# Kernel tuning notes

Measured on AMD Instinct MI355X. Metric: run time of the kernel, lower is better.

Reference implementation:

```python
import jax, jax.numpy as jnp
import numpy as np
from jax import lax

B, S, H, T = 64, 512, 1024, 48


def setup_inputs() -> dict:
    key = jax.random.key(0)
    ks = jax.random.split(key, 8)
    x = jax.random.normal(ks[0], (B, S, H), dtype=jnp.float32)
    # left-aligned variable-length attention mask (lengths in [S//2, S])
    lengths = jax.random.randint(ks[1], (B,), S // 2, S + 1)
    attention_mask = (jnp.arange(S)[None, :] < lengths[:, None]).astype(jnp.int32)
    labels = jax.random.randint(ks[2], (B, S), 0, T).astype(jnp.int64)
    # decoder Linear(H, T)
    W = jax.random.normal(ks[3], (H, T), dtype=jnp.float32) / np.sqrt(H)
    b = jnp.zeros((T,), dtype=jnp.float32)
    # CRF parameters (allennlp-style: transitions + start/end transitions)
    transitions = jax.random.normal(ks[4], (T, T), dtype=jnp.float32) * 0.1
    start_trans = jax.random.normal(ks[5], (T,), dtype=jnp.float32) * 0.1
    end_trans = jax.random.normal(ks[6], (T,), dtype=jnp.float32) * 0.1
    return {"x": x, "attention_mask": attention_mask, "labels": labels,
            "W": W, "b": b, "transitions": transitions,
            "start_trans": start_trans, "end_trans": end_trans}


def _log_partition(logits, mask, trans, start, end):
    # logits [B,S,T], mask [B,S] int. Returns logZ [B].
    alpha0 = start[None, :] + logits[:, 0]                     # [B,T]
    emits = jnp.moveaxis(logits[:, 1:], 1, 0)                  # [S-1,B,T]
    ms = mask[:, 1:].T                                         # [S-1,B]

    def step(alpha, inp):
        emit, m = inp
        inner = alpha[:, :, None] + trans[None, :, :] + emit[:, None, :]  # [B,T,T]
        new = jax.nn.logsumexp(inner, axis=1)
        alpha = jnp.where(m[:, None] > 0, new, alpha)
        return alpha, None

    alpha, _ = lax.scan(step, alpha0, (emits, ms))
    return jax.nn.logsumexp(alpha + end[None, :], axis=1)      # [B]


def _gold_score(logits, labels, mask, trans, start, end):
    maskf = mask.astype(logits.dtype)
    emit = jnp.take_along_axis(logits, labels[..., None], axis=2)[..., 0]  # [B,S]
    emit_score = jnp.sum(emit * maskf, axis=1)
    tr = trans[labels[:, :-1], labels[:, 1:]]                   # [B,S-1]
    trans_score = jnp.sum(tr * maskf[:, 1:], axis=1)
    last_idx = jnp.sum(mask, axis=1) - 1                        # [B]
    last_tags = jnp.take_along_axis(labels, last_idx[:, None], axis=1)[:, 0]
    return start[labels[:, 0]] + emit_score + trans_score + end[last_tags]


def _viterbi(logits, mask, trans, start, end):
    Bn, Sn, Tn = logits.shape
    v0 = start[None, :] + logits[:, 0]
    emits = jnp.moveaxis(logits[:, 1:], 1, 0)                  # [S-1,B,T]
    ms = mask[:, 1:].T
    ident = jnp.broadcast_to(jnp.arange(Tn, dtype=jnp.int32)[None, :], (Bn, Tn))

    def step(v, inp):
        emit, m = inp
        scores = v[:, :, None] + trans[None, :, :]              # [B,T_prev,T_cur]
        bp = jnp.argmax(scores, axis=1).astype(jnp.int32)       # [B,T]
        best = jnp.max(scores, axis=1) + emit
        v_new = jnp.where(m[:, None] > 0, best, v)
        bp = jnp.where(m[:, None] > 0, bp, ident)               # identity at padded steps
        return v_new, bp

    v, bps = lax.scan(step, v0, (emits, ms))                    # bps [S-1,B,T]
    last = jnp.argmax(v + end[None, :], axis=1).astype(jnp.int32)  # [B]

    def back(tag, bp):
        prev = jnp.take_along_axis(bp, tag[:, None], axis=1)[:, 0]
        return prev, tag

    first_tag, rest = lax.scan(back, last, bps, reverse=True)   # rest [S-1,B]
    tags = jnp.concatenate([first_tag[:, None], rest.T], axis=1)  # [B,S]
    return (tags * mask).astype(jnp.int64)                      # pad with zeros


def reference(x, attention_mask, labels, W, b, transitions, start_trans, end_trans):
    features = jnp.einsum('bsh,ht->bst', x, W) + b              # decoder Linear
    pred_labels = _viterbi(features, attention_mask, transitions, start_trans, end_trans)
    logZ = _log_partition(features, attention_mask, transitions, start_trans, end_trans)
    gold = _gold_score(features, labels, attention_mask, transitions, start_trans, end_trans)
    loss = -jnp.sum(gold - logZ)                                # -log-likelihood, summed over batch
    return features, pred_labels, loss
```

## Files before the change

### kernel.cpp

```cpp
#include <hip/hip_runtime.h>
#include <hip/hip_bf16.h>
#include <math.h>

#define Bn 64
#define Sn 512
#define Hn 1024
#define Tn 48

#define LOG2E 1.4426950408889634f
#define LN2f  0.6931471805599453f

#define PRED_OFF (Bn*Sn*Tn)
#define LOSS_OFF (PRED_OFF + Bn*Sn)

#define RL(x,i) __int_as_float(__builtin_amdgcn_readlane(__float_as_int(x),(i)))

#if __has_builtin(__builtin_amdgcn_exp2f)
#define EXP2(x) __builtin_amdgcn_exp2f(x)
#else
#define EXP2(x) exp2f(x)
#endif
#if __has_builtin(__builtin_amdgcn_logf)
#define LOG2(x) __builtin_amdgcn_logf(x)
#else
#define LOG2(x) log2f(x)
#endif

#define DOT4(ACC,A,B) { ACC += (A).x*(B).x; ACC += (A).y*(B).y; ACC += (A).z*(B).z; ACC += (A).w*(B).w; }

__global__ __launch_bounds__(256) void gemm_feat(
    const float* __restrict__ x, const float* __restrict__ W,
    const float* __restrict__ bias, float* __restrict__ feat)
{
  __shared__ __align__(16) float xs[128][68];
  __shared__ __align__(16) float wsT[Tn][68];
  const int tid = threadIdx.x;
  const int tx = tid & 7;
  const int ty = tid >> 3;
  const size_t row0 = (size_t)blockIdx.x * 128;
  const int srr = tid >> 4;
  const int scc = (tid & 15) * 4;

  float4 xreg[8];
  float  wreg[12];
  #pragma unroll
  for (int p = 0; p < 8; ++p)
    xreg[p] = *reinterpret_cast<const float4*>(&x[(row0 + srr + p*16)*Hn + scc]);
  #pragma unroll
  for (int i = 0; i < 12; ++i) {
    const int id = tid + i*256; const int kk = id/Tn; const int t = id - kk*Tn;
    wreg[i] = W[(size_t)kk*Tn + t];
  }

  float acc[4][6];
  #pragma unroll
  for (int r = 0; r < 4; ++r)
    #pragma unroll
    for (int c = 0; c < 6; ++c) acc[r][c] = 0.f;

  for (int k0 = 0; k0 < Hn; k0 += 64) {
    #pragma unroll
    for (int p = 0; p < 8; ++p)
      *reinterpret_cast<float4*>(&xs[srr + p*16][scc]) = xreg[p];
    #pragma unroll
    for (int i = 0; i < 12; ++i) {
      const int id = tid + i*256; const int kk = id/Tn; const int t = id - kk*Tn;
      wsT[t][kk] = wreg[i];
    }
    __syncthreads();
    if (k0 + 64 < Hn) {
      #pragma unroll
      for (int p = 0; p < 8; ++p)
        xreg[p] = *reinterpret_cast<const float4*>(&x[(row0 + srr + p*16)*Hn + (k0+64) + scc]);
      #pragma unroll
      for (int i = 0; i < 12; ++i) {
        const int id = tid + i*256; const int kk = id/Tn; const int t = id - kk*Tn;
        wreg[i] = W[(size_t)(k0 + 64 + kk)*Tn + t];
      }
    }
    #pragma unroll 4
    for (int kk = 0; kk < 64; kk += 4) {
      const float4 a0 = *reinterpret_cast<const float4*>(&xs[ty*4+0][kk]);
      const float4 a1 = *reinterpret_cast<const float4*>(&xs[ty*4+1][kk]);
      const float4 a2 = *reinterpret_cast<const float4*>(&xs[ty*4+2][kk]);
      const float4 a3 = *reinterpret_cast<const float4*>(&xs[ty*4+3][kk]);
      const float4 w0 = *reinterpret_cast<const float4*>(&wsT[tx*6+0][kk]);
      const float4 w1 = *reinterpret_cast<const float4*>(&wsT[tx*6+1][kk]);
      const float4 w2 = *reinterpret_cast<const float4*>(&wsT[tx*6+2][kk]);
      const float4 w3 = *reinterpret_cast<const float4*>(&wsT[tx*6+3][kk]);
      const float4 w4 = *reinterpret_cast<const float4*>(&wsT[tx*6+4][kk]);
      const float4 w5 = *reinterpret_cast<const float4*>(&wsT[tx*6+5][kk]);
      DOT4(acc[0][0],a0,w0) DOT4(acc[0][1],a0,w1) DOT4(acc[0][2],a0,w2)
      DOT4(acc[0][3],a0,w3) DOT4(acc[0][4],a0,w4) DOT4(acc[0][5],a0,w5)
      DOT4(acc[1][0],a1,w0) DOT4(acc[1][1],a1,w1) DOT4(acc[1][2],a1,w2)
      DOT4(acc[1][3],a1,w3) DOT4(acc[1][4],a1,w4) DOT4(acc[1][5],a1,w5)
      DOT4(acc[2][0],a2,w0) DOT4(acc[2][1],a2,w1) DOT4(acc[2][2],a2,w2)
      DOT4(acc[2][3],a2,w3) DOT4(acc[2][4],a2,w4) DOT4(acc[2][5],a2,w5)
      DOT4(acc[3][0],a3,w0) DOT4(acc[3][1],a3,w1) DOT4(acc[3][2],a3,w2)
      DOT4(acc[3][3],a3,w3) DOT4(acc[3][4],a3,w4) DOT4(acc[3][5],a3,w5)
    }
    __syncthreads();
  }
  #pragma unroll
  for (int c = 0; c < 6; ++c) {
    const int col = tx*6 + c;
    const float bv = bias[col];
    #pragma unroll
    for (int r = 0; r < 4; ++r)
      feat[(row0 + ty*4 + r)*Tn + col] = acc[r][c] + bv;
  }
}

__global__ __launch_bounds__(64, 1) void crf_kernel(
    const float* __restrict__ feat,
    const int* __restrict__ mask,
    const int* __restrict__ labels,
    const float* __restrict__ trans,
    const float* __restrict__ startv,
    const float* __restrict__ endv,
    float* __restrict__ pred_out,
    float* __restrict__ wsLogZ,
    float* __restrict__ wsGold)
{
  __shared__ unsigned char bpL[Sn*64];
  __shared__ unsigned char predL[Sn];

  const int role = blockIdx.x >> 6;
  const int b    = blockIdx.x & 63;
  const int lane = threadIdx.x;
  const float* fb = feat + (size_t)b * Sn * Tn;

  int lc = 0;
  #pragma unroll
  for (int it = 0; it < Sn/64; ++it) lc += (mask[(size_t)b*Sn + it*64 + lane] != 0);
  #pragma unroll
  for (int off = 32; off; off >>= 1) lc += __shfl_xor(lc, off);
  const int len = lc;

  const int j = (lane < Tn) ? lane : (Tn - 1);

  if (role == 0) {
    float4 trT[12];
    #pragma unroll
    for (int k = 0; k < 12; ++k) {
      trT[k].x = trans[(4*k+0)*Tn + j] * LOG2E;
      trT[k].y = trans[(4*k+1)*Tn + j] * LOG2E;
      trT[k].z = trans[(4*k+2)*Tn + j] * LOG2E;
      trT[k].w = trans[(4*k+3)*Tn + j] * LOG2E;
    }
    const float a0 = (startv[j] + fb[j]) * LOG2E;
    float Zref = RL(a0, 0);
    float beta = a0 - Zref;
    float em_cur = fb[Tn + j];
    for (int t = 1; t < len; ++t) {
      const int tn = (t + 1 < len) ? (t + 1) : t;
      const float em_nxt = fb[(size_t)tn*Tn + j];
      float s0 = 0.f, s1 = 0.f, s2 = 0.f, s3 = 0.f;
      #pragma unroll
      for (int k = 0; k < 12; ++k) {
        s0 += EXP2(RL(beta, 4*k+0) + trT[k].x);
        s1 += EXP2(RL(beta, 4*k+1) + trT[k].y);
        s2 += EXP2(RL(beta, 4*k+2) + trT[k].z);
        s3 += EXP2(RL(beta, 4*k+3) + trT[k].w);
      }
      const float dj = LOG2((s0 + s1) + (s2 + s3)) + em_cur * LOG2E;
      const float d0 = RL(dj, 0);
      Zref += d0;
      beta = dj - d0;
      em_cur = em_nxt;
    }
    float fv = (lane < Tn) ? beta + endv[lane] * LOG2E : -INFINITY;
    float m = fv;
    #pragma unroll
    for (int off = 32; off; off >>= 1) m = fmaxf(m, __shfl_xor(m, off));
    float e = (lane < Tn) ? EXP2(fv - m) : 0.f;
    #pragma unroll
    for (int off = 32; off; off >>= 1) e += __shfl_xor(e, off);
    if (lane == 0) wsLogZ[b] = (Zref + m + LOG2(e)) * LN2f;

  } else if (role == 1) {
    float4 trR[12];
    #pragma unroll
    for (int k = 0; k < 12; ++k) {
      trR[k].x = trans[(4*k+0)*Tn + j];
      trR[k].y = trans[(4*k+1)*Tn + j];
      trR[k].z = trans[(4*k+2)*Tn + j];
      trR[k].w = trans[(4*k+3)*Tn + j];
    }
    float v = startv[j] + fb[j];
    float em_cur = fb[Tn + j];
    for (int t = 1; t < len; ++t) {
      const int tn = (t + 1 < len) ? (t + 1) : t;
      const float em_nxt = fb[(size_t)tn*Tn + j];
      float bestA = -INFINITY, bestB = -INFINITY;
      int idxA = 0, idxB = 0;
      #pragma unroll
      for (int k = 0; k < 12; ++k) {
        const float4 tr = trR[k];
        const float q0 = RL(v, 4*k+0) + tr.x;
        const float q1 = RL(v, 4*k+1) + tr.y;
        const float q2 = RL(v, 4*k+2) + tr.z;
        const float q3 = RL(v, 4*k+3) + tr.w;
        float gv = q0; int gi = 4*k;
        bool g1 = q1 > gv; gv = g1 ? q1 : gv; gi = g1 ? 4*k+1 : gi;
        bool g2 = q2 > gv; gv = g2 ? q2 : gv; gi = g2 ? 4*k+2 : gi;
        bool g3 = q3 > gv; gv = g3 ? q3 : gv; gi = g3 ? 4*k+3 : gi;
        if ((k & 1) == 0) { bool g = gv > bestA; bestA = g ? gv : bestA; idxA = g ? gi : idxA; }
        else              { bool g = gv > bestB; bestB = g ? gv : bestB; idxB = g ? gi : idxB; }
      }
      float best; int bidx;
      if (bestB > bestA || (bestB == bestA && idxB < idxA)) { best = bestB; bidx = idxB; }
      else                                                  { best = bestA; bidx = idxA; }
      bpL[t*64 + lane] = (unsigned char)bidx;
      v = best + em_cur;
      em_cur = em_nxt;
    }
    float fv = (lane < Tn) ? v + endv[lane] : -INFINITY;
    int fi = (lane < Tn) ? lane : 64;
    #pragma unroll
    for (int off = 32; off; off >>= 1) {
      const float ov = __shfl_xor(fv, off);
      const int   oi = __shfl_xor(fi, off);
      if (ov > fv || (ov == fv && oi < fi)) { fv = ov; fi = oi; }
    }
    __syncthreads();
    if (lane == 0) {
      int tag = fi;
      predL[len - 1] = (unsigned char)tag;
      for (int t = len - 1; t >= 1; --t) {
        tag = bpL[t*64 + tag];
        predL[t - 1] = (unsigned char)tag;
      }
    }
    __syncthreads();
    #pragma unroll
    for (int it = 0; it < Sn/64; ++it) {
      const int s = it*64 + lane;
      pred_out[(size_t)b*Sn + s] = (s < len) ? (float)predL[s] : 0.f;
    }

  } else {
    float g = 0.f;
    #pragma unroll
    for (int it = 0; it < Sn/64; ++it) {
      const int sg = it*64 + lane;
      if (sg < len) {
        const int la = labels[(size_t)b*Sn + sg];
        float e = fb[(size_t)sg*Tn + la];
        if (sg > 0) e += trans[labels[(size_t)b*Sn + sg - 1]*Tn + la];
        g += e;
      }
    }
    #pragma unroll
    for (int off = 32; off; off >>= 1) g += __shfl_xor(g, off);
    if (lane == 0) {
      g += startv[labels[(size_t)b*Sn]] + endv[labels[(size_t)b*Sn + len - 1]];
      wsGold[b] = g;
    }
  }
}

__global__ void loss_reduce(const float* __restrict__ wsLogZ,
                            const float* __restrict__ wsGold,
                            float* __restrict__ out)
{
  const int lane = threadIdx.x;
  float v = wsLogZ[lane] - wsGold[lane];
  #pragma unroll
  for (int off = 32; off; off >>= 1) v += __shfl_xor(v, off);
  if (lane == 0) out[0] = v;
}

extern "C" void kernel_launch(void* const* d_in, const int* in_sizes, int n_in,
                              void* d_out, int out_size, void* d_ws, size_t ws_size,
                              hipStream_t stream) {
  const float* x      = (const float*)d_in[0];
  const int*   mask   = (const int*)  d_in[1];
  const int*   labels = (const int*)  d_in[2];
  const float* W      = (const float*)d_in[3];
  const float* bias   = (const float*)d_in[4];
  const float* trans  = (const float*)d_in[5];
  const float* startv = (const float*)d_in[6];
  const float* endv   = (const float*)d_in[7];

  float* out  = (float*)d_out;
  float* feat = out;
  float* pred = out + PRED_OFF;
  float* loss = out + LOSS_OFF;
  float* wsLogZ = (float*)d_ws;
  float* wsGold = wsLogZ + 64;

  gemm_feat<<<(Bn*Sn)/128, 256, 0, stream>>>(x, W, bias, feat);
  crf_kernel<<<192, 64, 0, stream>>>(feat, mask, labels, trans, startv, endv, pred, wsLogZ, wsGold);
  loss_reduce<<<1, 64, 0, stream>>>(wsLogZ, wsGold, loss);
}
```

Measured before the change: 386.0 us.

## Rewrite feature GEMM split-K, use exp-domain forward, parallel Viterbi backtrace

```diff
diff --git a/kernel.cpp b/kernel.cpp
--- a/kernel.cpp
+++ b/kernel.cpp
@@ -26,89 +26,76 @@
 #define LOG2(x) log2f(x)
 #endif
 
-#define DOT4(ACC,A,B) { ACC += (A).x*(B).x; ACC += (A).y*(B).y; ACC += (A).z*(B).z; ACC += (A).w*(B).w; }
+template<int CTRL>
+__device__ __forceinline__ float dpp_add(float v) {
+  return v + __int_as_float(__builtin_amdgcn_update_dpp(
+      0, __float_as_int(v), CTRL, 0xf, 0xf, false));
+}
 
 __global__ __launch_bounds__(256) void gemm_feat(
     const float* __restrict__ x, const float* __restrict__ W,
     const float* __restrict__ bias, float* __restrict__ feat)
 {
-  __shared__ __align__(16) float xs[128][68];
-  __shared__ __align__(16) float wsT[Tn][68];
   const int tid = threadIdx.x;
-  const int tx = tid & 7;
-  const int ty = tid >> 3;
-  const size_t row0 = (size_t)blockIdx.x * 128;
-  const int srr = tid >> 4;
-  const int scc = (tid & 15) * 4;
-
-  float4 xreg[8];
-  float  wreg[12];
-  #pragma unroll
-  for (int p = 0; p < 8; ++p)
-    xreg[p] = *reinterpret_cast<const float4*>(&x[(row0 + srr + p*16)*Hn + scc]);
-  #pragma unroll
-  for (int i = 0; i < 12; ++i) {
-    const int id = tid + i*256; const int kk = id/Tn; const int t = id - kk*Tn;
-    wreg[i] = W[(size_t)kk*Tn + t];
-  }
-
-  float acc[4][6];
-  #pragma unroll
-  for (int r = 0; r < 4; ++r)
-    #pragma unroll
-    for (int c = 0; c < 6; ++c) acc[r][c] = 0.f;
+  const int klane = tid & 15;
+  const int cg = tid >> 4;
+  const int col0 = cg * 3;
+  const size_t row0 = (size_t)blockIdx.x * 16;
+
+  float acc[16][3];
+  #pragma unroll
+  for (int r = 0; r < 16; ++r) { acc[r][0]=0.f; acc[r][1]=0.f; acc[r][2]=0.f; }
+
+  const float* xb = x + row0 * Hn + klane * 4;
+  const float* wb = W + (size_t)(klane * 4) * Tn + col0;
 
   for (int k0 = 0; k0 < Hn; k0 += 64) {
-    #pragma unroll
-    for (int p = 0; p < 8; ++p)
-      *reinterpret_cast<float4*>(&xs[srr + p*16][scc]) = xreg[p];
-    #pragma unroll
-    for (int i = 0; i < 12; ++i) {
-      const int id = tid + i*256; const int kk = id/Tn; const int t = id - kk*Tn;
-      wsT[t][kk] = wreg[i];
-    }
-    __syncthreads();
-    if (k0 + 64 < Hn) {
-      #pragma unroll
-      for (int p = 0; p < 8; ++p)
-        xreg[p] = *reinterpret_cast<const float4*>(&x[(row0 + srr + p*16)*Hn + (k0+64) + scc]);
-      #pragma unroll
-      for (int i = 0; i < 12; ++i) {
-        const int id = tid + i*256; const int kk = id/Tn; const int t = id - kk*Tn;
-        wreg[i] = W[(size_t)(k0 + 64 + kk)*Tn + t];
-      }
-    }
-    #pragma unroll 4
-    for (int kk = 0; kk < 64; kk += 4) {
-      const float4 a0 = *reinterpret_cast<const float4*>(&xs[ty*4+0][kk]);
-      const float4 a1 = *reinterpret_cast<const float4*>(&xs[ty*4+1][kk]);
-      const float4 a2 = *reinterpret_cast<const float4*>(&xs[ty*4+2][kk]);
-      const float4 a3 = *reinterpret_cast<const float4*>(&xs[ty*4+3][kk]);
-      const float4 w0 = *reinterpret_cast<const float4*>(&wsT[tx*6+0][kk]);
-      const float4 w1 = *reinterpret_cast<const float4*>(&wsT[tx*6+1][kk]);
-      const float4 w2 = *reinterpret_cast<const float4*>(&wsT[tx*6+2][kk]);
-      const float4 w3 = *reinterpret_cast<const float4*>(&wsT[tx*6+3][kk]);
-      const float4 w4 = *reinterpret_cast<const float4*>(&wsT[tx*6+4][kk]);
-      const float4 w5 = *reinterpret_cast<const float4*>(&wsT[tx*6+5][kk]);
-      DOT4(acc[0][0],a0,w0) DOT4(acc[0][1],a0,w1) DOT4(acc[0][2],a0,w2)
-      DOT4(acc[0][3],a0,w3) DOT4(acc[0][4],a0,w4) DOT4(acc[0][5],a0,w5)
-      DOT4(acc[1][0],a1,w0) DOT4(acc[1][1],a1,w1) DOT4(acc[1][2],a1,w2)
-      DOT4(acc[1][3],a1,w3) DOT4(acc[1][4],a1,w4) DOT4(acc[1][5],a1,w5)
-      DOT4(acc[2][0],a2,w0) DOT4(acc[2][1],a2,w1) DOT4(acc[2][2],a2,w2)
-      DOT4(acc[2][3],a2,w3) DOT4(acc[2][4],a2,w4) DOT4(acc[2][5],a2,w5)
-      DOT4(acc[3][0],a3,w0) DOT4(acc[3][1],a3,w1) DOT4(acc[3][2],a3,w2)
-      DOT4(acc[3][3],a3,w3) DOT4(acc[3][4],a3,w4) DOT4(acc[3][5],a3,w5)
-    }
-    __syncthreads();
-  }
-  #pragma unroll
-  for (int c = 0; c < 6; ++c) {
-    const int col = tx*6 + c;
-    const float bv = bias[col];
-    #pragma unroll
-    for (int r = 0; r < 4; ++r)
-      feat[(row0 + ty*4 + r)*Tn + col] = acc[r][c] + bv;
-  }
+    float w[3][4];
+    #pragma unroll
+    for (int kk = 0; kk < 4; ++kk) {
+      #pragma unroll
+      for (int c = 0; c < 3; ++c)
+        w[c][kk] = wb[(size_t)(k0 + kk) * Tn + c];
+    }
+    float4 a[16];
+    #pragma unroll
+    for (int r = 0; r < 16; ++r)
+      a[r] = *reinterpret_cast<const float4*>(&xb[(size_t)r * Hn + k0]);
+    #pragma unroll
+    for (int r = 0; r < 16; ++r) {
+      #pragma unroll
+      for (int c = 0; c < 3; ++c) {
+        acc[r][c] = fmaf(a[r].x, w[c][0], acc[r][c]);
+        acc[r][c] = fmaf(a[r].y, w[c][1], acc[r][c]);
+        acc[r][c] = fmaf(a[r].z, w[c][2], acc[r][c]);
+        acc[r][c] = fmaf(a[r].w, w[c][3], acc[r][c]);
+      }
+    }
+  }
+  #pragma unroll
+  for (int r = 0; r < 16; ++r) {
+    #pragma unroll
+    for (int c = 0; c < 3; ++c) {
+      float v = acc[r][c];
+      v = dpp_add<0x128>(v);
+      v = dpp_add<0x124>(v);
+      v = dpp_add<0x122>(v);
+      v = dpp_add<0x121>(v);
+      acc[r][c] = v;
+    }
+  }
+  float o0 = acc[0][0], o1 = acc[0][1], o2 = acc[0][2];
+  #pragma unroll
+  for (int r = 1; r < 16; ++r) {
+    const bool sel = (klane == r);
+    o0 = sel ? acc[r][0] : o0;
+    o1 = sel ? acc[r][1] : o1;
+    o2 = sel ? acc[r][2] : o2;
+  }
+  float* fo = feat + (row0 + klane) * Tn + col0;
+  fo[0] = o0 + bias[col0 + 0];
+  fo[1] = o1 + bias[col0 + 1];
+  fo[2] = o2 + bias[col0 + 2];
 }
 
 __global__ __launch_bounds__(64, 1) void crf_kernel(
@@ -122,8 +109,9 @@
     float* __restrict__ wsLogZ,
     float* __restrict__ wsGold)
 {
-  __shared__ unsigned char bpL[Sn*64];
-  __shared__ unsigned char predL[Sn];
+  __shared__ unsigned char bpL[Sn * 64];
+  __shared__ unsigned char pathL[384 * 64];
+  __shared__ int EA[8];
 
   const int role = blockIdx.x >> 6;
   const int b    = blockIdx.x & 63;
@@ -140,34 +128,30 @@
   const int j = (lane < Tn) ? lane : (Tn - 1);
 
   if (role == 0) {
-    float4 trT[12];
-    #pragma unroll
-    for (int k = 0; k < 12; ++k) {
-      trT[k].x = trans[(4*k+0)*Tn + j] * LOG2E;
-      trT[k].y = trans[(4*k+1)*Tn + j] * LOG2E;
-      trT[k].z = trans[(4*k+2)*Tn + j] * LOG2E;
-      trT[k].w = trans[(4*k+3)*Tn + j] * LOG2E;
-    }
+    float Ev[48];
+    #pragma unroll
+    for (int i = 0; i < 48; ++i) Ev[i] = EXP2(trans[i*Tn + j] * LOG2E);
     const float a0 = (startv[j] + fb[j]) * LOG2E;
     float Zref = RL(a0, 0);
     float beta = a0 - Zref;
-    float em_cur = fb[Tn + j];
+    float em2 = fb[Tn + j] * LOG2E;
     for (int t = 1; t < len; ++t) {
       const int tn = (t + 1 < len) ? (t + 1) : t;
-      const float em_nxt = fb[(size_t)tn*Tn + j];
-      float s0 = 0.f, s1 = 0.f, s2 = 0.f, s3 = 0.f;
-      #pragma unroll
-      for (int k = 0; k < 12; ++k) {
-        s0 += EXP2(RL(beta, 4*k+0) + trT[k].x);
-        s1 += EXP2(RL(beta, 4*k+1) + trT[k].y);
-        s2 += EXP2(RL(beta, 4*k+2) + trT[k].z);
-        s3 += EXP2(RL(beta, 4*k+3) + trT[k].w);
-      }
-      const float dj = LOG2((s0 + s1) + (s2 + s3)) + em_cur * LOG2E;
+      const float em_nxt = fb[(size_t)tn*Tn + j] * LOG2E;
+      const float p = EXP2(beta);
+      float s0=0.f, s1=0.f, s2=0.f, s3=0.f;
+      #pragma unroll
+      for (int i = 0; i < 48; i += 4) {
+        s0 = fmaf(RL(p, i+0), Ev[i+0], s0);
+        s1 = fmaf(RL(p, i+1), Ev[i+1], s1);
+        s2 = fmaf(RL(p, i+2), Ev[i+2], s2);
+        s3 = fmaf(RL(p, i+3), Ev[i+3], s3);
+      }
+      const float dj = LOG2((s0 + s1) + (s2 + s3)) + em2;
       const float d0 = RL(dj, 0);
       Zref += d0;
       beta = dj - d0;
-      em_cur = em_nxt;
+      em2 = em_nxt;
     }
     float fv = (lane < Tn) ? beta + endv[lane] * LOG2E : -INFINITY;
     float m = fv;
@@ -179,42 +163,37 @@
     if (lane == 0) wsLogZ[b] = (Zref + m + LOG2(e)) * LN2f;
 
   } else if (role == 1) {
-    float4 trR[12];
-    #pragma unroll
-    for (int k = 0; k < 12; ++k) {
-      trR[k].x = trans[(4*k+0)*Tn + j];
-      trR[k].y = trans[(4*k+1)*Tn + j];
-      trR[k].z = trans[(4*k+2)*Tn + j];
-      trR[k].w = trans[(4*k+3)*Tn + j];
-    }
+    float trv[48];
+    #pragma unroll
+    for (int i = 0; i < 48; ++i) trv[i] = trans[i*Tn + j];
     float v = startv[j] + fb[j];
     float em_cur = fb[Tn + j];
     for (int t = 1; t < len; ++t) {
       const int tn = (t + 1 < len) ? (t + 1) : t;
       const float em_nxt = fb[(size_t)tn*Tn + j];
-      float bestA = -INFINITY, bestB = -INFINITY;
-      int idxA = 0, idxB = 0;
-      #pragma unroll
-      for (int k = 0; k < 12; ++k) {
-        const float4 tr = trR[k];
-        const float q0 = RL(v, 4*k+0) + tr.x;
-        const float q1 = RL(v, 4*k+1) + tr.y;
-        const float q2 = RL(v, 4*k+2) + tr.z;
-        const float q3 = RL(v, 4*k+3) + tr.w;
-        float gv = q0; int gi = 4*k;
-        bool g1 = q1 > gv; gv = g1 ? q1 : gv; gi = g1 ? 4*k+1 : gi;
-        bool g2 = q2 > gv; gv = g2 ? q2 : gv; gi = g2 ? 4*k+2 : gi;
-        bool g3 = q3 > gv; gv = g3 ? q3 : gv; gi = g3 ? 4*k+3 : gi;
-        if ((k & 1) == 0) { bool g = gv > bestA; bestA = g ? gv : bestA; idxA = g ? gi : idxA; }
-        else              { bool g = gv > bestB; bestB = g ? gv : bestB; idxB = g ? gi : idxB; }
-      }
-      float best; int bidx;
-      if (bestB > bestA || (bestB == bestA && idxB < idxA)) { best = bestB; bidx = idxB; }
-      else                                                  { best = bestA; bidx = idxA; }
-      bpL[t*64 + lane] = (unsigned char)bidx;
+      float q[48];
+      #pragma unroll
+      for (int i = 0; i < 48; ++i) q[i] = RL(v, i) + trv[i];
+      float m16[16];
+      #pragma unroll
+      for (int u = 0; u < 16; ++u)
+        m16[u] = fmaxf(fmaxf(q[3*u], q[3*u+1]), q[3*u+2]);
+      float n0 = fmaxf(fmaxf(m16[0],m16[1]),m16[2]);
+      float n1 = fmaxf(fmaxf(m16[3],m16[4]),m16[5]);
+      float n2 = fmaxf(fmaxf(m16[6],m16[7]),m16[8]);
+      float n3 = fmaxf(fmaxf(m16[9],m16[10]),m16[11]);
+      float n4 = fmaxf(fmaxf(m16[12],m16[13]),m16[14]);
+      float n5 = m16[15];
+      const float best = fmaxf(fmaxf(fmaxf(n0,n1),fmaxf(n2,n3)), fmaxf(n4,n5));
+      int idx = 47;
+      #pragma unroll
+      for (int i = 46; i >= 0; --i) idx = (q[i] == best) ? i : idx;
+      bpL[t*64 + lane] = (unsigned char)idx;
       v = best + em_cur;
       em_cur = em_nxt;
     }
+    for (int t = len; t < Sn; ++t) bpL[t*64 + lane] = (unsigned char)lane;
+
     float fv = (lane < Tn) ? v + endv[lane] : -INFINITY;
     int fi = (lane < Tn) ? lane : 64;
     #pragma unroll
@@ -224,19 +203,41 @@
       if (ov > fv || (ov == fv && oi < fi)) { fv = ov; fi = oi; }
     }
     __syncthreads();
+
+    #define JOB(r) \
+      const int id##r  = lane + 64*(r); \
+      const int seg##r = id##r & 7;     \
+      int cur##r = id##r >> 3;          \
+      const int bpb##r = seg##r << 12;  \
+      const int pb##r  = id##r << 6;    \
+      pathL[pb##r + 63] = (unsigned char)cur##r;
+    JOB(0) JOB(1) JOB(2) JOB(3) JOB(4) JOB(5)
+    for (int d = 62; d >= 0; --d) {
+      const int o = (d + 1) << 6;
+      cur0 = bpL[bpb0 + o + cur0]; pathL[pb0 + d] = (unsigned char)cur0;
+      cur1 = bpL[bpb1 + o + cur1]; pathL[pb1 + d] = (unsigned char)cur1;
+      cur2 = bpL[bpb2 + o + cur2]; pathL[pb2 + d] = (unsigned char)cur2;
+      cur3 = bpL[bpb3 + o + cur3]; pathL[pb3 + d] = (unsigned char)cur3;
+      cur4 = bpL[bpb4 + o + cur4]; pathL[pb4 + d] = (unsigned char)cur4;
+      cur5 = bpL[bpb5 + o + cur5]; pathL[pb5 + d] = (unsigned char)cur5;
+    }
+    #undef JOB
+    __syncthreads();
     if (lane == 0) {
-      int tag = fi;
-      predL[len - 1] = (unsigned char)tag;
-      for (int t = len - 1; t >= 1; --t) {
-        tag = bpL[t*64 + tag];
-        predL[t - 1] = (unsigned char)tag;
+      int Ecur = fi;
+      EA[7] = Ecur;
+      for (int s = 7; s >= 1; --s) {
+        const int bottom = pathL[((Ecur << 3) + s) * 64];
+        Ecur = bpL[(s << 12) + bottom];
+        EA[s-1] = Ecur;
       }
     }
     __syncthreads();
     #pragma unroll
-    for (int it = 0; it < Sn/64; ++it) {
-      const int s = it*64 + lane;
-      pred_out[(size_t)b*Sn + s] = (s < len) ? (float)predL[s] : 0.f;
+    for (int r8 = 0; r8 < 8; ++r8) {
+      const int t = r8*64 + lane;
+      const int pv = pathL[((EA[r8] << 3) + r8) * 64 + lane];
+      pred_out[(size_t)b*Sn + t] = (t < len) ? (float)pv : 0.f;
     }
 
   } else {
@@ -290,7 +291,7 @@
   float* wsLogZ = (float*)d_ws;
   float* wsGold = wsLogZ + 64;
 
-  gemm_feat<<<(Bn*Sn)/128, 256, 0, stream>>>(x, W, bias, feat);
+  gemm_feat<<<(Bn*Sn)/16, 256, 0, stream>>>(x, W, bias, feat);
   crf_kernel<<<192, 64, 0, stream>>>(feat, mask, labels, trans, startv, endv, pred, wsLogZ, wsGold);
   loss_reduce<<<1, 64, 0, stream>>>(wsLogZ, wsGold, loss);
 }
```

Result: slower. 432.0 us (+11.9%).
